# Kernel optimization log

Hardware: AMD Instinct MI355X
Metric: run time of the kernel (lower is better)

## Reference

```python
import math
import jax, jax.numpy as jnp
import numpy as np

B, T, S = 2, 2048, 2048
D_MODEL, N_HEADS = 1024, 16
HEAD_DIM = D_MODEL // N_HEADS
OUT_DIM = 1024


def setup_inputs() -> dict:
    key = jax.random.key(0)
    ks = jax.random.split(key, 6)
    q = jax.random.normal(ks[0], (B, T, D_MODEL), dtype=jnp.float32)
    k = jax.random.normal(ks[1], (B, S, D_MODEL), dtype=jnp.float32)
    v = jax.random.normal(ks[2], (B, S, D_MODEL), dtype=jnp.float32)
    rel_pos_bias = jax.random.normal(ks[3], (T, S, N_HEADS), dtype=jnp.float32)
    # shared qkv projection weight (torch ModuleList([Linear]*3) aliases one module)
    lim = 1.0 / math.sqrt(D_MODEL)
    Wqkv = jax.random.uniform(ks[4], (D_MODEL, D_MODEL), minval=-lim, maxval=lim, dtype=jnp.float32)
    Wout = jax.random.uniform(ks[5], (OUT_DIM, D_MODEL), minval=-lim, maxval=lim, dtype=jnp.float32)
    logit_scale = jnp.full((N_HEADS, 1, 1), math.log(10.0), dtype=jnp.float32)
    return {"q": q, "k": k, "v": v, "rel_pos_bias": rel_pos_bias,
            "Wqkv": Wqkv, "Wout": Wout, "logit_scale": logit_scale}


def _l2norm(x, eps=1e-12):
    # matches torch F.normalize(dim=-1)
    n = jnp.sqrt(jnp.sum(x * x, axis=-1, keepdims=True))
    return x / jnp.maximum(n, eps)


def reference(q, k, v, rel_pos_bias, Wqkv, Wout, logit_scale):
    # shared qkv projection (Linear, no bias): x @ W.T
    qp = q @ Wqkv.T
    kp = k @ Wqkv.T
    vp = v @ Wqkv.T
    # [B, H, T, Dh]
    qh = qp.reshape(B, T, N_HEADS, HEAD_DIM).transpose(0, 2, 1, 3)
    kh = kp.reshape(B, S, N_HEADS, HEAD_DIM).transpose(0, 2, 1, 3)
    vh = vp.reshape(B, S, N_HEADS, HEAD_DIM).transpose(0, 2, 1, 3)
    # cosine attention with clamped learned logit scale
    scale = jnp.exp(jnp.minimum(logit_scale, math.log(100.0)))  # [H,1,1]
    attn = jnp.einsum('bhtd,bhsd->bhts', _l2norm(qh), _l2norm(kh)) * scale
    # rel_pos_bias [T,S,H] -> [H,T,S], broadcast over batch
    attn = attn + rel_pos_bias.transpose(2, 0, 1)
    attn = jax.nn.softmax(attn, axis=-1)
    vals = jnp.einsum('bhts,bhsd->bhtd', attn, vh)
    vals = vals.transpose(0, 2, 1, 3).reshape(B, T, D_MODEL)
    return vals @ Wout.T
```

## Files before the change

### kernel.cpp

```cpp
#include <hip/hip_runtime.h>
#include <stdint.h>

typedef unsigned short u16;
using bf16x8 = __attribute__((ext_vector_type(8))) __bf16;
using f32x4  = __attribute__((ext_vector_type(4))) float;
using u16x8  = __attribute__((ext_vector_type(8))) u16;
using u16x4  = __attribute__((ext_vector_type(4))) u16;
using i32x4  = __attribute__((ext_vector_type(4))) int;

#define BB 2
#define TT 2048
#define SQ 2048
#define DM 1024
#define NH 16
#define HD 64
#define LOG2E 1.44269504088896340736f

__device__ __forceinline__ float bf2f(u16 u) {
  uint32_t x = ((uint32_t)u) << 16;
  return __builtin_bit_cast(float, x);
}
__device__ __forceinline__ u16 f2bf(float f) {
  uint32_t x = __builtin_bit_cast(uint32_t, f);
  x += 0x7fffu + ((x >> 16) & 1u);
  return (u16)(x >> 16);
}
__device__ __forceinline__ int cvt_pk_bf16(float lo, float hi) {
  int r;
  asm("v_cvt_pk_bf16_f32 %0, %1, %2" : "=v"(r) : "v"(lo), "v"(hi));
  return r;
}

typedef __attribute__((address_space(1))) void gvoid;
typedef __attribute__((address_space(3))) void lvoid;
__device__ __forceinline__ void g2l16(const void* g, void* l) {
  __builtin_amdgcn_global_load_lds((gvoid*)g, (lvoid*)l, 16, 0, 0);
}

__global__ __launch_bounds__(256) void convert_all(
    const float* __restrict__ q, const float* __restrict__ k,
    const float* __restrict__ v, const float* __restrict__ wq,
    const float* __restrict__ wo, u16* __restrict__ qc, u16* __restrict__ kc,
    u16* __restrict__ vc, u16* __restrict__ wqc, u16* __restrict__ woc) {
  const float* src;
  u16* dst;
  int n8;
  switch (blockIdx.y) {
    case 0:  src = q;  dst = qc;  n8 = 4096 * 1024 / 8; break;
    case 1:  src = k;  dst = kc;  n8 = 4096 * 1024 / 8; break;
    case 2:  src = v;  dst = vc;  n8 = 4096 * 1024 / 8; break;
    case 3:  src = wq; dst = wqc; n8 = 1024 * 1024 / 8; break;
    default: src = wo; dst = woc; n8 = 1024 * 1024 / 8; break;
  }
  int i = blockIdx.x * 256 + threadIdx.x;
  if (i >= n8) return;
  f32x4 a = ((const f32x4*)src)[(size_t)i * 2];
  f32x4 b = ((const f32x4*)src)[(size_t)i * 2 + 1];
  u16x8 o;
#pragma unroll
  for (int j = 0; j < 4; ++j) { o[j] = f2bf(a[j]); o[4 + j] = f2bf(b[j]); }
  ((u16x8*)dst)[i] = o;
}

template <typename OutT>
__device__ __forceinline__ void gemm_body(const u16* __restrict__ A,
                                          const u16* __restrict__ W,
                                          OutT* __restrict__ C,
                                          const float* __restrict__ ls,
                                          int norm_mode) {
  const int n0 = blockIdx.x * 128;
  const int m0 = blockIdx.y * 128;
  const int tid = threadIdx.x;
  const int w = tid >> 6, lane = tid & 63;
  const int l15 = lane & 15, lg = lane >> 4;
  const int wr = w >> 1, wc = w & 1;

  __shared__ u16 ldsA[16 * 512];
  __shared__ u16 ldsB[16 * 512];

  f32x4 acc[4][4];
#pragma unroll
  for (int i = 0; i < 4; ++i)
#pragma unroll
    for (int j = 0; j < 4; ++j) acc[i][j] = (f32x4){0.f, 0.f, 0.f, 0.f};

  for (int kt = 0; kt < 1024; kt += 64) {
#pragma unroll
    for (int u = 0; u < 4; ++u) {
      int f = w * 4 + u;
      int mt = f >> 1, ks = f & 1;
      g2l16(A + (size_t)(m0 + mt * 16 + l15) * 1024 + kt + ks * 32 + lg * 8,
            &ldsA[f * 512]);
      g2l16(W + (size_t)(n0 + mt * 16 + l15) * 1024 + kt + ks * 32 + lg * 8,
            &ldsB[f * 512]);
    }
    __syncthreads();
#pragma unroll
    for (int ks = 0; ks < 2; ++ks) {
      bf16x8 a[4], b[4];
#pragma unroll
      for (int i = 0; i < 4; ++i)
        a[i] = *(const bf16x8*)&ldsA[((wr * 4 + i) * 2 + ks) * 512 + lane * 8];
#pragma unroll
      for (int j = 0; j < 4; ++j)
        b[j] = *(const bf16x8*)&ldsB[((wc * 4 + j) * 2 + ks) * 512 + lane * 8];
#pragma unroll
      for (int i = 0; i < 4; ++i)
#pragma unroll
        for (int j = 0; j < 4; ++j)
          acc[i][j] = __builtin_amdgcn_mfma_f32_16x16x32_bf16(a[i], b[j],
                                                              acc[i][j], 0, 0, 0);
    }
    __syncthreads();
  }

  if (norm_mode < 2) {
    float sc = 1.0f;
    if (norm_mode == 0)
      sc = __expf(fminf(ls[(n0 >> 6) + wc], 4.60517019f)) * LOG2E;
#pragma unroll
    for (int i = 0; i < 4; ++i)
#pragma unroll
      for (int r = 0; r < 4; ++r) {
        float ss = 0.f;
#pragma unroll
        for (int j = 0; j < 4; ++j) ss += acc[i][j][r] * acc[i][j][r];
#pragma unroll
        for (int d = 1; d < 16; d <<= 1) ss += __shfl_xor(ss, d, 64);
        float f = sc / fmaxf(sqrtf(ss), 1e-12f);
#pragma unroll
        for (int j = 0; j < 4; ++j) acc[i][j][r] *= f;
      }
  }

#pragma unroll
  for (int i = 0; i < 4; ++i) {
    int row0 = m0 + (wr * 4 + i) * 16 + lg * 4;
#pragma unroll
    for (int j = 0; j < 4; ++j) {
      int col = n0 + (wc * 4 + j) * 16 + l15;
#pragma unroll
      for (int r = 0; r < 4; ++r) {
        if constexpr (sizeof(OutT) == 2)
          C[(size_t)(row0 + r) * 1024 + col] = f2bf(acc[i][j][r]);
        else
          C[(size_t)(row0 + r) * 1024 + col] = acc[i][j][r];
      }
    }
  }
}

__global__ __launch_bounds__(256, 2) void gemm_qkv(
    const u16* __restrict__ q, const u16* __restrict__ k,
    const u16* __restrict__ v, const u16* __restrict__ W,
    const float* __restrict__ ls,
    u16* __restrict__ qp, u16* __restrict__ kp, u16* __restrict__ vp) {
  const u16* A;
  u16* C;
  if (blockIdx.z == 0) { A = q; C = qp; }
  else if (blockIdx.z == 1) { A = k; C = kp; }
  else { A = v; C = vp; }
  gemm_body<u16>(A, W, C, ls, blockIdx.z);
}

__global__ __launch_bounds__(256, 2) void gemm_out(const u16* __restrict__ A,
                                                   const u16* __restrict__ W,
                                                   float* __restrict__ C) {
  gemm_body<float>(A, W, C, nullptr, 2);
}

__global__ __launch_bounds__(256) void transpose_v(const u16* __restrict__ vp,
                                                   u16* __restrict__ vt) {
  int st = blockIdx.x;
  int bh = blockIdx.y;
  __shared__ u16 lds[64][72];
  int tid = threadIdx.x;
  int s = tid >> 2, c0 = (tid & 3) * 16;
  int b = bh >> 4, h = bh & 15;
  const u16* src = vp + (size_t)(b * SQ + st * 64 + s) * 1024 + h * 64 + c0;
  u16x8 r0 = *(const u16x8*)src;
  u16x8 r1 = *(const u16x8*)(src + 8);
#pragma unroll
  for (int j = 0; j < 8; ++j) { lds[s][c0 + j] = r0[j]; lds[s][c0 + 8 + j] = r1[j]; }
  __syncthreads();
  int d = tid >> 2, sc = (tid & 3) * 16;
  u16x8 o0, o1;
#pragma unroll
  for (int j = 0; j < 8; ++j) { o0[j] = lds[sc + j][d]; o1[j] = lds[sc + 8 + j][d]; }
  u16* dst = vt + (size_t)(bh * 64 + d) * SQ + st * 64 + sc;
  *(u16x8*)dst = o0;
  *((u16x8*)(dst + 8)) = o1;
}

__global__ __launch_bounds__(256) void transpose_bias(const float* __restrict__ bias,
                                                      u16* __restrict__ bt) {
  int t = blockIdx.y;
  int s0 = blockIdx.x * 512;
  __shared__ u16 lds[16][520];
  int tid = threadIdx.x;
  const float* src = bias + ((size_t)t * SQ + s0) * 16;
  int h0 = (tid & 3) * 4;
  int sr = tid >> 2;
#pragma unroll
  for (int p = 0; p < 8; ++p) {
    f32x4 r = *(const f32x4*)(src + p * 1024 + tid * 4);
#pragma unroll
    for (int e = 0; e < 4; ++e)
      lds[h0 + e][p * 64 + sr] = f2bf(r[e] * LOG2E);
  }
  __syncthreads();
  int h = tid >> 4, sc = (tid & 15) * 32;
  u16* dst = bt + ((size_t)h * TT + t) * SQ + s0 + sc;
#pragma unroll
  for (int j = 0; j < 4; ++j) {
    u16x8 o;
#pragma unroll
    for (int e = 0; e < 8; ++e) o[e] = lds[h][sc + j * 8 + e];
    *((u16x8*)(dst + j * 8)) = o;
  }
}

__global__ __launch_bounds__(512, 2) void flash_attn(
    const u16* __restrict__ qn, const u16* __restrict__ kn,
    const u16* __restrict__ vt, const u16* __restrict__ bt,
    u16* __restrict__ av) {
  const int h = blockIdx.x, qt = blockIdx.y;
  const int tid = threadIdx.x, lane = tid & 63;
  const int wAll = tid >> 6;
  const int b = wAll >> 2, w = wAll & 3;
  const int l15 = lane & 15, lg = lane >> 4;

  __shared__ u16 ldsK[2][2][16 * 512];
  __shared__ u16 ldsV[2][2][16 * 512];

  const int t0 = qt * 64 + w * 16;

  bf16x8 qf[2];
  {
    const u16* qb = qn + (size_t)(b * TT + t0 + l15) * 1024 + h * 64 + lg * 8;
    qf[0] = *(const bf16x8*)qb;
    qf[1] = *(const bf16x8*)(qb + 32);
  }

  f32x4 o[4];
#pragma unroll
  for (int n = 0; n < 4; ++n) o[n] = (f32x4){0.f, 0.f, 0.f, 0.f};
  float li = 0.f;

  const u16* kb = kn + (size_t)(b * SQ) * 1024 + h * 64;
  const u16* vb = vt + (size_t)((b * NH + h) * 64) * SQ;
  const u16* bbl = bt + ((size_t)h * TT + t0 + l15) * SQ + lg * 4;

#define STAGE(bufi, stg)                                                       \
  {                                                                            \
    _Pragma("unroll") for (int u_ = 0; u_ < 4; ++u_) {                         \
      int f_ = w * 4 + u_;                                                     \
      int nt_ = f_ >> 1, ks_ = f_ & 1;                                         \
      g2l16(kb + (size_t)((stg) + nt_ * 16 + l15) * 1024 + ks_ * 32 + lg * 8,  \
            &ldsK[bufi][b][f_ * 512]);                                         \
      int j_ = f_ >> 2, k2_ = f_ & 3;                                          \
      g2l16(vb + (size_t)(j_ * 16 + l15) * SQ + (stg) + k2_ * 32 + lg * 8,     \
            &ldsV[bufi][b][f_ * 512]);                                         \
    }                                                                          \
  }

  STAGE(0, 0);

  for (int it = 0; it < 16; ++it) {
    const int cur = it & 1;
    const int st = it * 128;

    u16x4 bv[8];
#pragma unroll
    for (int nt = 0; nt < 8; ++nt)
      bv[nt] = *(const u16x4*)(bbl + st + nt * 16);
    asm volatile("" ::: "memory");

    if (it < 15) {
      STAGE(cur ^ 1, st + 128);
      asm volatile("s_waitcnt vmcnt(16)" ::: "memory");
    } else {
      asm volatile("s_waitcnt vmcnt(8)" ::: "memory");
    }
    __builtin_amdgcn_s_barrier();

    f32x4 sacc[8];
#pragma unroll
    for (int nt = 0; nt < 8; ++nt) {
      sacc[nt] = (f32x4){0.f, 0.f, 0.f, 0.f};
#pragma unroll
      for (int ks = 0; ks < 2; ++ks)
        sacc[nt] = __builtin_amdgcn_mfma_f32_16x16x32_bf16(
            *(const bf16x8*)&ldsK[cur][b][(nt * 2 + ks) * 512 + lane * 8],
            qf[ks], sacc[nt], 0, 0, 0);
    }

    int pk[8][2];
#pragma unroll
    for (int nt = 0; nt < 8; ++nt) {
      float p0 = __builtin_amdgcn_exp2f(sacc[nt][0] + bf2f(bv[nt][0]));
      float p1 = __builtin_amdgcn_exp2f(sacc[nt][1] + bf2f(bv[nt][1]));
      float p2 = __builtin_amdgcn_exp2f(sacc[nt][2] + bf2f(bv[nt][2]));
      float p3 = __builtin_amdgcn_exp2f(sacc[nt][3] + bf2f(bv[nt][3]));
      li += (p0 + p1) + (p2 + p3);
      pk[nt][0] = cvt_pk_bf16(p0, p1);
      pk[nt][1] = cvt_pk_bf16(p2, p3);
    }

#pragma unroll
    for (int ks2 = 0; ks2 < 4; ++ks2) {
      auto a0 = __builtin_amdgcn_permlane32_swap(pk[2 * ks2][0],
                                                 pk[2 * ks2 + 1][0], false, false);
      auto w0 = __builtin_amdgcn_permlane16_swap(a0[0], a0[1], false, false);
      auto a1 = __builtin_amdgcn_permlane32_swap(pk[2 * ks2][1],
                                                 pk[2 * ks2 + 1][1], false, false);
      auto w1 = __builtin_amdgcn_permlane16_swap(a1[0], a1[1], false, false);
      i32x4 pw = (i32x4){(int)w0[0], (int)w1[0], (int)w0[1], (int)w1[1]};
      bf16x8 pf = __builtin_bit_cast(bf16x8, pw);
#pragma unroll
      for (int j = 0; j < 4; ++j)
        o[j] = __builtin_amdgcn_mfma_f32_16x16x32_bf16(
            pf, *(const bf16x8*)&ldsV[cur][b][(j * 4 + ks2) * 512 + lane * 8],
            o[j], 0, 0, 0);
    }
    if (it < 15) __builtin_amdgcn_s_barrier();
  }
#undef STAGE

  li += __shfl_xor(li, 16, 64);
  li += __shfl_xor(li, 32, 64);
  float inv[4];
#pragma unroll
  for (int r = 0; r < 4; ++r) inv[r] = 1.0f / __shfl(li, lg * 4 + r, 64);

#pragma unroll
  for (int j = 0; j < 4; ++j)
#pragma unroll
    for (int r = 0; r < 4; ++r) {
      size_t row = (size_t)(b * TT + t0 + lg * 4 + r);
      av[row * 1024 + h * 64 + j * 16 + l15] = f2bf(o[j][r] * inv[r]);
    }
}

extern "C" void kernel_launch(void* const* d_in, const int* in_sizes, int n_in,
                              void* d_out, int out_size, void* d_ws, size_t ws_size,
                              hipStream_t stream) {
  const float* q    = (const float*)d_in[0];
  const float* k    = (const float*)d_in[1];
  const float* v    = (const float*)d_in[2];
  const float* bias = (const float*)d_in[3];
  const float* Wqkv = (const float*)d_in[4];
  const float* Wout = (const float*)d_in[5];
  const float* ls   = (const float*)d_in[6];
  float* out = (float*)d_out;

  char* ws = (char*)d_ws;
  u16* qc = (u16*)(ws);
  u16* kc = (u16*)(ws + (size_t)(8  << 20));
  u16* vc = (u16*)(ws + (size_t)(16 << 20));
  u16* Wq = (u16*)(ws + (size_t)(24 << 20));
  u16* Wo = (u16*)(ws + (size_t)(26 << 20));
  u16* qn = (u16*)(ws + (size_t)(28 << 20));
  u16* kn = (u16*)(ws + (size_t)(36 << 20));
  u16* av = (u16*)(ws + (size_t)(44 << 20));
  u16* vtb = (u16*)(ws + (size_t)(52 << 20));
  u16* bt  = (u16*)(ws + (size_t)(60 << 20));

  dim3 blk(256);
  transpose_bias<<<dim3(4, 2048), blk, 0, stream>>>(bias, bt);
  convert_all<<<dim3(2048, 5), blk, 0, stream>>>(q, k, v, Wqkv, Wout,
                                                 qc, kc, vc, Wq, Wo);

  gemm_qkv<<<dim3(8, 32, 3), blk, 0, stream>>>(qc, kc, vc, Wq, ls, qn, kn, av);
  transpose_v<<<dim3(32, 32), blk, 0, stream>>>(av, vtb);
  flash_attn<<<dim3(16, 32), dim3(512), 0, stream>>>(qn, kn, vtb, bt, av);
  gemm_out<<<dim3(8, 32), blk, 0, stream>>>(av, Wo, out);
}
```

Baseline: 672.7 us.

## Split flash attention blocks per batch with smaller KV tiles and MFMA priority

The attention kernel moves from 512-thread blocks covering both batches to 256-thread blocks with one (batch, head) pair each. The KV tile shrinks from 128 to 64 keys, so LDS per block is roughly a quarter and the loop runs twice as many iterations. Wave priority is raised around the MFMA sections. The aim is more resident blocks per CU and finer scheduling, at the cost of more barriers and loop overhead and less K/V reuse per staging step.

```diff
diff --git a/kernel.cpp b/kernel.cpp
--- a/kernel.cpp
+++ b/kernel.cpp
@@ -220,18 +220,16 @@
   }
 }
 
-__global__ __launch_bounds__(512, 2) void flash_attn(
+__global__ __launch_bounds__(256, 4) void flash_attn(
     const u16* __restrict__ qn, const u16* __restrict__ kn,
     const u16* __restrict__ vt, const u16* __restrict__ bt,
     u16* __restrict__ av) {
-  const int h = blockIdx.x, qt = blockIdx.y;
-  const int tid = threadIdx.x, lane = tid & 63;
-  const int wAll = tid >> 6;
-  const int b = wAll >> 2, w = wAll & 3;
+  const int h = blockIdx.x & 15, b = blockIdx.x >> 4, qt = blockIdx.y;
+  const int tid = threadIdx.x, w = tid >> 6, lane = tid & 63;
   const int l15 = lane & 15, lg = lane >> 4;
 
-  __shared__ u16 ldsK[2][2][16 * 512];
-  __shared__ u16 ldsV[2][2][16 * 512];
+  __shared__ u16 ldsK[2][8 * 512];
+  __shared__ u16 ldsV[2][8 * 512];
 
   const int t0 = qt * 64 + w * 16;
 
@@ -255,49 +253,55 @@
   {                                                                            \
     _Pragma("unroll") for (int u_ = 0; u_ < 4; ++u_) {                         \
       int f_ = w * 4 + u_;                                                     \
-      int nt_ = f_ >> 1, ks_ = f_ & 1;                                         \
-      g2l16(kb + (size_t)((stg) + nt_ * 16 + l15) * 1024 + ks_ * 32 + lg * 8,  \
-            &ldsK[bufi][b][f_ * 512]);                                         \
-      int j_ = f_ >> 2, k2_ = f_ & 3;                                          \
-      g2l16(vb + (size_t)(j_ * 16 + l15) * SQ + (stg) + k2_ * 32 + lg * 8,     \
-            &ldsV[bufi][b][f_ * 512]);                                         \
+      if (f_ < 8) {                                                            \
+        int nt_ = f_ >> 1, ks_ = f_ & 1;                                       \
+        g2l16(kb + (size_t)((stg) + nt_ * 16 + l15) * 1024 + ks_ * 32 + lg * 8,\
+              &ldsK[bufi][f_ * 512]);                                          \
+      } else {                                                                 \
+        int f2_ = f_ - 8;                                                      \
+        int j_ = f2_ >> 1, k2_ = f2_ & 1;                                      \
+        g2l16(vb + (size_t)(j_ * 16 + l15) * SQ + (stg) + k2_ * 32 + lg * 8,   \
+              &ldsV[bufi][f2_ * 512]);                                         \
+      }                                                                        \
     }                                                                          \
   }
 
   STAGE(0, 0);
 
-  for (int it = 0; it < 16; ++it) {
+  for (int it = 0; it < 32; ++it) {
     const int cur = it & 1;
-    const int st = it * 128;
-
-    u16x4 bv[8];
-#pragma unroll
-    for (int nt = 0; nt < 8; ++nt)
+    const int st = it * 64;
+
+    u16x4 bv[4];
+#pragma unroll
+    for (int nt = 0; nt < 4; ++nt)
       bv[nt] = *(const u16x4*)(bbl + st + nt * 16);
     asm volatile("" ::: "memory");
 
-    if (it < 15) {
-      STAGE(cur ^ 1, st + 128);
-      asm volatile("s_waitcnt vmcnt(16)" ::: "memory");
+    if (it < 31) {
+      STAGE(cur ^ 1, st + 64);
+      asm volatile("s_waitcnt vmcnt(8)" ::: "memory");
     } else {
-      asm volatile("s_waitcnt vmcnt(8)" ::: "memory");
+      asm volatile("s_waitcnt vmcnt(4)" ::: "memory");
     }
     __builtin_amdgcn_s_barrier();
 
-    f32x4 sacc[8];
-#pragma unroll
-    for (int nt = 0; nt < 8; ++nt) {
+    f32x4 sacc[4];
+    __builtin_amdgcn_s_setprio(1);
+#pragma unroll
+    for (int nt = 0; nt < 4; ++nt) {
       sacc[nt] = (f32x4){0.f, 0.f, 0.f, 0.f};
 #pragma unroll
       for (int ks = 0; ks < 2; ++ks)
         sacc[nt] = __builtin_amdgcn_mfma_f32_16x16x32_bf16(
-            *(const bf16x8*)&ldsK[cur][b][(nt * 2 + ks) * 512 + lane * 8],
+            *(const bf16x8*)&ldsK[cur][(nt * 2 + ks) * 512 + lane * 8],
             qf[ks], sacc[nt], 0, 0, 0);
     }
-
-    int pk[8][2];
-#pragma unroll
-    for (int nt = 0; nt < 8; ++nt) {
+    __builtin_amdgcn_s_setprio(0);
+
+    int pk[4][2];
+#pragma unroll
+    for (int nt = 0; nt < 4; ++nt) {
       float p0 = __builtin_amdgcn_exp2f(sacc[nt][0] + bf2f(bv[nt][0]));
       float p1 = __builtin_amdgcn_exp2f(sacc[nt][1] + bf2f(bv[nt][1]));
       float p2 = __builtin_amdgcn_exp2f(sacc[nt][2] + bf2f(bv[nt][2]));
@@ -308,7 +312,7 @@
     }
 
 #pragma unroll
-    for (int ks2 = 0; ks2 < 4; ++ks2) {
+    for (int ks2 = 0; ks2 < 2; ++ks2) {
       auto a0 = __builtin_amdgcn_permlane32_swap(pk[2 * ks2][0],
                                                  pk[2 * ks2 + 1][0], false, false);
       auto w0 = __builtin_amdgcn_permlane16_swap(a0[0], a0[1], false, false);
@@ -317,13 +321,15 @@
       auto w1 = __builtin_amdgcn_permlane16_swap(a1[0], a1[1], false, false);
       i32x4 pw = (i32x4){(int)w0[0], (int)w1[0], (int)w0[1], (int)w1[1]};
       bf16x8 pf = __builtin_bit_cast(bf16x8, pw);
+      __builtin_amdgcn_s_setprio(1);
 #pragma unroll
       for (int j = 0; j < 4; ++j)
         o[j] = __builtin_amdgcn_mfma_f32_16x16x32_bf16(
-            pf, *(const bf16x8*)&ldsV[cur][b][(j * 4 + ks2) * 512 + lane * 8],
+            pf, *(const bf16x8*)&ldsV[cur][(j * 2 + ks2) * 512 + lane * 8],
             o[j], 0, 0, 0);
-    }
-    if (it < 15) __builtin_amdgcn_s_barrier();
+      __builtin_amdgcn_s_setprio(0);
+    }
+    if (it < 31) __builtin_amdgcn_s_barrier();
   }
 #undef STAGE
 
@@ -373,6 +379,6 @@
 
   gemm_qkv<<<dim3(8, 32, 3), blk, 0, stream>>>(qc, kc, vc, Wq, ls, qn, kn, av);
   transpose_v<<<dim3(32, 32), blk, 0, stream>>>(av, vtb);
-  flash_attn<<<dim3(16, 32), dim3(512), 0, stream>>>(qn, kn, vtb, bt, av);
+  flash_attn<<<dim3(32, 32), blk, 0, stream>>>(qn, kn, vtb, bt, av);
   gemm_out<<<dim3(8, 32), blk, 0, stream>>>(av, Wo, out);
 }
```

New measurement: 647.7 us. 1.04x faster.
